# Kernel optimization log

Measured on AMD Instinct MI355X. Metric: run time of the kernel, lower is better.

Reference implementation:

```python
import jax, jax.numpy as jnp
import numpy as np
from jax import lax

B, S, V, E, H = 128, 48, 20000, 620, 2400


def setup_inputs() -> dict:
    key = jax.random.key(0)
    ks = jax.random.split(key, 13)
    s = 0.05
    return {
        "tokens": jax.random.randint(ks[0], (B, S), 0, V),
        "lengths": jax.random.randint(ks[1], (B,), 1, S + 1),
        "emb": jax.random.normal(ks[2], (V, E), jnp.float32) * s,
        "W_ir": jax.random.normal(ks[3], (H, E), jnp.float32) * s,
        "W_ii": jax.random.normal(ks[4], (H, E), jnp.float32) * s,
        "W_in": jax.random.normal(ks[5], (H, E), jnp.float32) * s,
        "b_ir": jax.random.normal(ks[6], (H,), jnp.float32) * s,
        "b_ii": jax.random.normal(ks[7], (H,), jnp.float32) * s,
        "b_in": jax.random.normal(ks[8], (H,), jnp.float32) * s,
        "W_hr": jax.random.normal(ks[9], (H, H), jnp.float32) * s,
        "W_hi": jax.random.normal(ks[10], (H, H), jnp.float32) * s,
        "W_hn": jax.random.normal(ks[11], (H, H), jnp.float32) * s,
    }


def reference(tokens, lengths, emb, W_ir, W_ii, W_in, b_ir, b_ii, b_in, W_hr, W_hi, W_hn):
    x = emb[tokens]  # [B,S,E]
    # Precompute all input-side projections (batched GEMMs): [B,S,H]
    xr = jnp.einsum('bse,he->bsh', x, W_ir) + b_ir
    xi = jnp.einsum('bse,he->bsh', x, W_ii) + b_ii
    xn = jnp.einsum('bse,he->bsh', x, W_in) + b_in

    def step(h, xs):
        xr_t, xi_t, xn_t = xs  # each [B,H]
        r = jax.nn.sigmoid(xr_t + h @ W_hr.T)
        i = jax.nn.sigmoid(xi_t + h @ W_hi.T)
        n = jnp.tanh(xn_t + r * (h @ W_hn.T))
        h_new = (1.0 - i) * n + i * h
        return h_new, h_new

    h0 = jnp.zeros((B, H), x.dtype)
    xs = (xr.swapaxes(0, 1), xi.swapaxes(0, 1), xn.swapaxes(0, 1))  # [S,B,H]
    _, outs = lax.scan(step, h0, xs)
    outs = outs.swapaxes(0, 1)  # [B,S,H]
    # return_last=True: pick hidden at position lengths-1 (mask-mul + sum == gather)
    idx = jnp.clip(lengths - 1, 0, S - 1)
    last = jnp.take_along_axis(outs, idx[:, None, None], axis=1).squeeze(1)  # [B,H]
    return last
```

## Files before the change

### kernel.cpp

```cpp
#include <hip/hip_runtime.h>
#include <stdint.h>
#include <stddef.h>

#define B_  128
#define S_  48
#define E_  620
#define EP  640
#define H_  2400
#define N3  7200
#define KH  2400
#define P1_ITERS 20
#define KZ   5
#define KZI  15
#define UG   48
#define NG   50
#define WCHUNK 512
#define WIT    (9 * WCHUNK)
#define ACH    4096

typedef _Float16 half_t;
typedef __attribute__((ext_vector_type(8))) _Float16 half8;
typedef __attribute__((ext_vector_type(4))) _Float16 half4;
typedef __attribute__((ext_vector_type(4))) float    floatx4;

__device__ __forceinline__ void lds_barrier() {
  __builtin_amdgcn_sched_barrier(0);
  __builtin_amdgcn_s_waitcnt(0xC07F);
  __builtin_amdgcn_s_barrier();
  __builtin_amdgcn_sched_barrier(0);
}

__global__ void gather_cast_x(const int* __restrict__ tokens,
                              const float* __restrict__ emb,
                              half_t* __restrict__ xb) {
  int idx = blockIdx.x * 256 + threadIdx.x;
  int m = idx / EP, c = idx - m * EP;
  float v = 0.f;
  if (c < E_) v = emb[(size_t)tokens[m] * E_ + c];
  xb[idx] = (half_t)v;
}

__global__ void convert_wi(const float* __restrict__ Wir, const float* __restrict__ Wii,
                           const float* __restrict__ Win,
                           const float* __restrict__ bir, const float* __restrict__ bii,
                           const float* __restrict__ bin,
                           half_t* __restrict__ Wi, float* __restrict__ bias) {
  int idx = blockIdx.x * 256 + threadIdx.x;
  int r = idx / EP, c = idx - r * EP;
  const float* W = (r < H_) ? Wir : (r < 2*H_ ? Wii : Win);
  int rr = (r < H_) ? r : (r < 2*H_ ? r - H_ : r - 2*H_);
  float v = (c < E_) ? W[(size_t)rr * E_ + c] : 0.f;
  Wi[idx] = (half_t)v;
  if (c == 0) {
    const float* bb = (r < H_) ? bir : (r < 2*H_ ? bii : bin);
    bias[r] = bb[rr];
  }
}

__global__ void convert_wh(const float* __restrict__ Whr, const float* __restrict__ Whi,
                           const float* __restrict__ Whn, half_t* __restrict__ Wp) {
  int idx = blockIdx.x * 256 + threadIdx.x;
  int r3 = idx / KH, c = idx - r3 * KH;
  const float* W = (r3 < H_) ? Whr : (r3 < 2*H_ ? Whi : Whn);
  int p  = (r3 < H_) ? 0 : (r3 < 2*H_ ? 1 : 2);
  int rr = r3 - p * H_;
  int g = rr / UG, u = rr - g * UG;
  int nw = u >> 4, fm = u & 15;
  int kz = c / 480, kt = (c - kz * 480) >> 5, ksub = c & 31;
  size_t chunk = ((size_t)(g * KZ + kz) * KZI + kt) * 9 + (nw * 3 + p);
  size_t dst = chunk * WCHUNK + ((ksub >> 3) * 16 + fm) * 8 + (ksub & 7);
  Wp[dst] = (half_t)W[(size_t)rr * KH + c];
}

__global__ void init_h(float* __restrict__ h, half_t* __restrict__ Ap) {
  int idx = blockIdx.x * 256 + threadIdx.x;
  h[idx] = 0.f;
  Ap[idx] = (half_t)0.f;
}

__global__ __launch_bounds__(256, 4) void gemm_x(
    const half_t* __restrict__ A,
    const half_t* __restrict__ Bm,
    half_t* __restrict__ C,
    const float* __restrict__ bias)
{
  __shared__ half_t As[2][4096];
  __shared__ half_t Bs[2][4096];

  const int tid = threadIdx.x;
  const int lane = tid & 63;
  const int w = tid >> 6;
  const int m0 = blockIdx.x * 128;
  const int n0 = blockIdx.y * 128;
  const int wm = (w >> 1) * 64, wn = (w & 1) * 64;

  const int c0 = tid, c1 = tid + 256;
  const int rA0 = m0 + (c0 >> 6) * 16 + (c0 & 15), q0 = ((c0 >> 4) & 3) * 8;
  const int rA1 = m0 + (c1 >> 6) * 16 + (c1 & 15), q1 = ((c1 >> 4) & 3) * 8;
  int rB0 = n0 + (c0 >> 6) * 16 + (c0 & 15); if (rB0 >= N3) rB0 = N3 - 1;
  int rB1 = n0 + (c1 >> 6) * 16 + (c1 & 15); if (rB1 >= N3) rB1 = N3 - 1;
  const half_t* pA0 = A  + (size_t)rA0 * EP + q0;
  const half_t* pA1 = A  + (size_t)rA1 * EP + q1;
  const half_t* pB0 = Bm + (size_t)rB0 * EP + q0;
  const half_t* pB1 = Bm + (size_t)rB1 * EP + q1;

  floatx4 acc[4][4] = {};

  half8 ga0 = *(const half8*)(pA0);
  half8 ga1 = *(const half8*)(pA1);
  half8 gb0 = *(const half8*)(pB0);
  half8 gb1 = *(const half8*)(pB1);
  *(half8*)(As[0] + c0 * 8) = ga0;
  *(half8*)(As[0] + c1 * 8) = ga1;
  *(half8*)(Bs[0] + c0 * 8) = gb0;
  *(half8*)(Bs[0] + c1 * 8) = gb1;
  ga0 = *(const half8*)(pA0 + 32);
  ga1 = *(const half8*)(pA1 + 32);
  gb0 = *(const half8*)(pB0 + 32);
  gb1 = *(const half8*)(pB1 + 32);
  lds_barrier();

  #pragma unroll
  for (int i = 0; i < P1_ITERS; ++i) {
    const int cur = i & 1, nxt = cur ^ 1;
    half8 a[4], b[4];
    #pragma unroll
    for (int f = 0; f < 4; ++f) {
      a[f] = *(const half8*)(As[cur] + (((wm >> 4) + f) * 64 + lane) * 8);
      b[f] = *(const half8*)(Bs[cur] + (((wn >> 4) + f) * 64 + lane) * 8);
    }
    if (i + 1 < P1_ITERS) {
      *(half8*)(As[nxt] + c0 * 8) = ga0;
      *(half8*)(As[nxt] + c1 * 8) = ga1;
      *(half8*)(Bs[nxt] + c0 * 8) = gb0;
      *(half8*)(Bs[nxt] + c1 * 8) = gb1;
    }
    if (i + 2 < P1_ITERS) {
      int ko = (i + 2) * 32;
      ga0 = *(const half8*)(pA0 + ko);
      ga1 = *(const half8*)(pA1 + ko);
      gb0 = *(const half8*)(pB0 + ko);
      gb1 = *(const half8*)(pB1 + ko);
    }
    #pragma unroll
    for (int mf = 0; mf < 4; ++mf)
      #pragma unroll
      for (int nf = 0; nf < 4; ++nf)
        acc[mf][nf] = __builtin_amdgcn_mfma_f32_16x16x32_f16(
            a[mf], b[nf], acc[mf][nf], 0, 0, 0);
    if (i + 1 < P1_ITERS) lds_barrier();
  }

  const int col = lane & 15, qr = (lane >> 4) * 4;
  #pragma unroll
  for (int nf = 0; nf < 4; ++nf) {
    int n = n0 + wn + nf * 16 + col;
    if (n >= N3) continue;
    float bv = bias[n];
    #pragma unroll
    for (int mf = 0; mf < 4; ++mf)
      #pragma unroll
      for (int r = 0; r < 4; ++r)
        C[(size_t)(m0 + wm + mf * 16 + qr + r) * N3 + n] =
            (half_t)(acc[mf][nf][r] + bv);
  }
}

__global__ __launch_bounds__(768, 3) void gru_gemm(
    const half_t* __restrict__ Ap_old,
    const half_t* __restrict__ Wp,
    half_t* __restrict__ Gp)
{
  __shared__ half_t S[3][8704];

  const int tid  = threadIdx.x;
  const int lane = tid & 63;
  const int w    = tid >> 6;
  const int mw   = w & 3;
  const int nw   = w >> 2;
  const int g    = blockIdx.x;
  const int kz   = blockIdx.y;

  const half_t* Asrc = Ap_old + (size_t)kz * KZI * ACH;
  const half_t* Wsrc = Wp + (size_t)(g * KZ + kz) * KZI * WIT;

  const bool isA  = tid < 512;
  const bool has1 = tid < 320;
  const half_t* sb0 = isA ? (Asrc + tid * 8) : (Wsrc + (tid - 512) * 8);
  const int     st0 = isA ? ACH : WIT;
  const half_t* sb1 = Wsrc + (tid + 256) * 8;
  const int d0 = tid * 8;
  const int d1 = ACH + (tid + 256) * 8;

  half8 p0 = *(const half8*)(sb0);
  half8 q0{}; if (has1) q0 = *(const half8*)(sb1);
  half8 p1 = *(const half8*)(sb0 + st0);
  half8 q1{}; if (has1) q1 = *(const half8*)(sb1 + WIT);
  *(half8*)(&S[0][d0]) = p0;  if (has1) *(half8*)(&S[0][d1]) = q0;
  *(half8*)(&S[1][d0]) = p1;  if (has1) *(half8*)(&S[1][d1]) = q1;
  half8 rp0 = *(const half8*)(sb0 + 2 * (size_t)st0);
  half8 rq0{}; if (has1) rq0 = *(const half8*)(sb1 + 2 * (size_t)WIT);
  half8 rp1 = *(const half8*)(sb0 + 3 * (size_t)st0);
  half8 rq1{}; if (has1) rq1 = *(const half8*)(sb1 + 3 * (size_t)WIT);
  lds_barrier();

  floatx4 acc[2][3] = {};
  const int aoff0 = (mw * 2 + 0) * 512 + lane * 8;
  const int aoff1 = (mw * 2 + 1) * 512 + lane * 8;
  const int woff  = ACH + nw * 3 * 512 + lane * 8;

  #pragma unroll
  for (int i = 0; i < KZI; ++i) {
    const int cur = i % 3, wb = (i + 2) % 3;
    half8 a0 = *(const half8*)(&S[cur][aoff0]);
    half8 a1 = *(const half8*)(&S[cur][aoff1]);
    half8 b0 = *(const half8*)(&S[cur][woff]);
    half8 b1 = *(const half8*)(&S[cur][woff + 512]);
    half8 b2 = *(const half8*)(&S[cur][woff + 1024]);
    if (i + 2 < KZI) {
      *(half8*)(&S[wb][d0]) = rp0;
      if (has1) *(half8*)(&S[wb][d1]) = rq0;
    }
    rp0 = rp1; rq0 = rq1;
    if (i + 4 < KZI) {
      rp1 = *(const half8*)(sb0 + (size_t)(i + 4) * st0);
      if (has1) rq1 = *(const half8*)(sb1 + (size_t)(i + 4) * WIT);
    }
    acc[0][0] = __builtin_amdgcn_mfma_f32_16x16x32_f16(a0, b0, acc[0][0], 0, 0, 0);
    acc[1][0] = __builtin_amdgcn_mfma_f32_16x16x32_f16(a1, b0, acc[1][0], 0, 0, 0);
    acc[0][1] = __builtin_amdgcn_mfma_f32_16x16x32_f16(a0, b1, acc[0][1], 0, 0, 0);
    acc[1][1] = __builtin_amdgcn_mfma_f32_16x16x32_f16(a1, b1, acc[1][1], 0, 0, 0);
    acc[0][2] = __builtin_amdgcn_mfma_f32_16x16x32_f16(a0, b2, acc[0][2], 0, 0, 0);
    acc[1][2] = __builtin_amdgcn_mfma_f32_16x16x32_f16(a1, b2, acc[1][2], 0, 0, 0);
    if (i + 1 < KZI) lds_barrier();
  }

  const int j  = g * UG + nw * 16 + (lane & 15);
  const int wm = mw * 32;
  const int qr = (lane >> 4) * 4;
  #pragma unroll
  for (int mf = 0; mf < 2; ++mf)
    #pragma unroll
    for (int p = 0; p < 3; ++p)
      #pragma unroll
      for (int r = 0; r < 4; ++r) {
        const int b = wm + mf * 16 + qr + r;
        Gp[((size_t)(kz * B_ + b) * 3 + p) * H_ + j] = (half_t)acc[mf][p][r];
      }
}

__global__ void gru_gate(
    const half_t* __restrict__ Gp,
    const half_t* __restrict__ gx,
    const float* __restrict__ hold,
    float* __restrict__ hnew,
    half_t* __restrict__ Ap_new,
    const int* __restrict__ lengths,
    float* __restrict__ out,
    int t)
{
  const int idx = blockIdx.x * 256 + threadIdx.x;
  const int b = idx / 600;
  const int j = (idx - b * 600) * 4;

  floatx4 G[3] = {};
  #pragma unroll
  for (int kz = 0; kz < KZ; ++kz)
    #pragma unroll
    for (int p = 0; p < 3; ++p) {
      half4 v = *(const half4*)(Gp + ((size_t)(kz * B_ + b) * 3 + p) * H_ + j);
      #pragma unroll
      for (int e = 0; e < 4; ++e) G[p][e] += (float)v[e];
    }

  const size_t rx = ((size_t)b * S_ + t) * N3 + j;
  half4 hxr = *(const half4*)(gx + rx);
  half4 hxi = *(const half4*)(gx + rx + H_);
  half4 hxn = *(const half4*)(gx + rx + 2 * H_);
  floatx4 ho = *(const floatx4*)(hold + (size_t)b * H_ + j);

  floatx4 hv4;
  half4 ap4;
  #pragma unroll
  for (int e = 0; e < 4; ++e) {
    const float rg = 1.f / (1.f + __expf(-((float)hxr[e] + G[0][e])));
    const float ig = 1.f / (1.f + __expf(-((float)hxi[e] + G[1][e])));
    const float ta = (float)hxn[e] + rg * G[2][e];
    const float nn = 1.f - 2.f / (1.f + __expf(2.f * ta));
    hv4[e] = (1.f - ig) * nn + ig * ho[e];
    ap4[e] = (half_t)hv4[e];
  }
  *(floatx4*)(hnew + (size_t)b * H_ + j) = hv4;

  const int kt = j >> 5, ksub = j & 31;
  const int mwb = b >> 5, rb = b & 31, mfb = rb >> 4, fmb = rb & 15;
  const size_t pos = (size_t)kt * ACH + (mwb * 2 + mfb) * 512
                   + ((ksub >> 3) * 16 + fmb) * 8 + (ksub & 7);
  *(half4*)(Ap_new + pos) = ap4;

  int lc = lengths[b] - 1;
  lc = lc < 0 ? 0 : (lc > S_ - 1 ? S_ - 1 : lc);
  if (t == lc) *(floatx4*)(out + (size_t)b * H_ + j) = hv4;
}

extern "C" void kernel_launch(void* const* d_in, const int* in_sizes, int n_in,
                              void* d_out, int out_size, void* d_ws, size_t ws_size,
                              hipStream_t stream)
{
  const int*   tokens  = (const int*)d_in[0];
  const int*   lengths = (const int*)d_in[1];
  const float* emb = (const float*)d_in[2];
  const float* Wir = (const float*)d_in[3];
  const float* Wii = (const float*)d_in[4];
  const float* Win = (const float*)d_in[5];
  const float* bir = (const float*)d_in[6];
  const float* bii = (const float*)d_in[7];
  const float* bin = (const float*)d_in[8];
  const float* Whr = (const float*)d_in[9];
  const float* Whi = (const float*)d_in[10];
  const float* Whn = (const float*)d_in[11];
  float* out = (float*)d_out;

  char* ws = (char*)d_ws;
  size_t off = 0;
  auto alloc = [&](size_t bytes) {
    void* p = ws + off;
    off = (off + bytes + 255) & ~(size_t)255;
    return p;
  };
  half_t* xb   = (half_t*)alloc((size_t)(B_ * S_) * EP * 2);
  half_t* Wi   = (half_t*)alloc((size_t)N3 * EP * 2);
  half_t* Wp   = (half_t*)alloc((size_t)N3 * KH * 2);
  float*  bias = (float*)alloc((size_t)N3 * 4);
  half_t* gx   = (half_t*)alloc((size_t)(B_ * S_) * N3 * 2);
  half_t* Gp   = (half_t*)alloc((size_t)KZ * B_ * N3 * 2);
  float*  h0   = (float*)alloc((size_t)B_ * H_ * 4);
  float*  h1   = (float*)alloc((size_t)B_ * H_ * 4);
  half_t* Ap0  = (half_t*)alloc((size_t)B_ * H_ * 2);
  half_t* Ap1  = (half_t*)alloc((size_t)B_ * H_ * 2);

  gather_cast_x<<<(B_ * S_ * EP) / 256, 256, 0, stream>>>(tokens, emb, xb);
  convert_wi<<<(N3 * EP) / 256, 256, 0, stream>>>(Wir, Wii, Win, bir, bii, bin, Wi, bias);
  convert_wh<<<(N3 * KH) / 256, 256, 0, stream>>>(Whr, Whi, Whn, Wp);
  init_h<<<(B_ * H_) / 256, 256, 0, stream>>>(h0, Ap0);

  gemm_x<<<dim3(48, 57), 256, 0, stream>>>(xb, Wi, gx, bias);

  for (int t = 0; t < S_; ++t) {
    const half_t* ai = (t & 1) ? Ap1 : Ap0;
    half_t*       aw = (t & 1) ? Ap0 : Ap1;
    const float*  ho = (t & 1) ? h1  : h0;
    float*        hn = (t & 1) ? h0  : h1;
    gru_gemm<<<dim3(NG, KZ), 768, 0, stream>>>(ai, Wp, Gp);
    gru_gate<<<(B_ * H_ / 4) / 256, 256, 0, stream>>>(
        Gp, gx, ho, hn, aw, lengths, out, t);
  }
}
```

Before: 1.041 ms.

## Pre-tile input GEMM operands and vectorize conversion and output stores

The conversion kernels now write x and the input weights directly in the per-tile fragment order that gemm_x uses, so each tile's loads become contiguous 16-byte reads instead of strided row gathers. The conversion kernels also process 8 elements per thread with half8 stores, including the recurrent-weight packing. gemm_x's epilogue stages results through shared memory so the output can be written as coalesced half8 rows instead of scattered 2-byte stores. The cost is a larger LDS footprint and an extra staging pass with barriers.

```diff
diff --git a/kernel.cpp b/kernel.cpp
--- a/kernel.cpp
+++ b/kernel.cpp
@@ -17,6 +17,7 @@
 #define WCHUNK 512
 #define WIT    (9 * WCHUNK)
 #define ACH    4096
+#define NBP  57
 
 typedef _Float16 half_t;
 typedef __attribute__((ext_vector_type(8))) _Float16 half8;
@@ -30,46 +31,70 @@
   __builtin_amdgcn_sched_barrier(0);
 }
 
+__device__ __forceinline__ int umap(int mr, int c0) {
+  return ((mr >> 4) << 6) | (((c0 & 31) >> 3) << 4) | (mr & 15);
+}
+
 __global__ void gather_cast_x(const int* __restrict__ tokens,
                               const float* __restrict__ emb,
-                              half_t* __restrict__ xb) {
+                              half_t* __restrict__ xp) {
   int idx = blockIdx.x * 256 + threadIdx.x;
-  int m = idx / EP, c = idx - m * EP;
-  float v = 0.f;
-  if (c < E_) v = emb[(size_t)tokens[m] * E_ + c];
-  xb[idx] = (half_t)v;
+  int m = idx / 80;
+  int c0 = (idx - m * 80) * 8;
+  int tok = tokens[m];
+  half8 v{};
+  #pragma unroll
+  for (int e = 0; e < 8; ++e) {
+    int c = c0 + e;
+    v[e] = (half_t)((c < E_) ? emb[(size_t)tok * E_ + c] : 0.f);
+  }
+  int mb = m >> 7, mr = m & 127, kt = c0 >> 5;
+  *(half8*)(xp + ((size_t)(mb * P1_ITERS + kt) * 512 + umap(mr, c0)) * 8) = v;
 }
 
 __global__ void convert_wi(const float* __restrict__ Wir, const float* __restrict__ Wii,
                            const float* __restrict__ Win,
                            const float* __restrict__ bir, const float* __restrict__ bii,
                            const float* __restrict__ bin,
-                           half_t* __restrict__ Wi, float* __restrict__ bias) {
+                           half_t* __restrict__ Wip, float* __restrict__ bias) {
   int idx = blockIdx.x * 256 + threadIdx.x;
-  int r = idx / EP, c = idx - r * EP;
-  const float* W = (r < H_) ? Wir : (r < 2*H_ ? Wii : Win);
-  int rr = (r < H_) ? r : (r < 2*H_ ? r - H_ : r - 2*H_);
-  float v = (c < E_) ? W[(size_t)rr * E_ + c] : 0.f;
-  Wi[idx] = (half_t)v;
-  if (c == 0) {
-    const float* bb = (r < H_) ? bir : (r < 2*H_ ? bii : bin);
-    bias[r] = bb[rr];
-  }
+  int r = idx / 80;
+  int c0 = (idx - r * 80) * 8;
+  half8 v{};
+  if (r < N3) {
+    const float* W = (r < H_) ? Wir : (r < 2*H_ ? Wii : Win);
+    int rr = (r < H_) ? r : (r < 2*H_ ? r - H_ : r - 2*H_);
+    #pragma unroll
+    for (int e = 0; e < 8; ++e) {
+      int c = c0 + e;
+      v[e] = (half_t)((c < E_) ? W[(size_t)rr * E_ + c] : 0.f);
+    }
+    if (c0 == 0) {
+      const float* bb = (r < H_) ? bir : (r < 2*H_ ? bii : bin);
+      bias[r] = bb[rr];
+    }
+  }
+  int nb = r >> 7, mr = r & 127, kt = c0 >> 5;
+  *(half8*)(Wip + ((size_t)(nb * P1_ITERS + kt) * 512 + umap(mr, c0)) * 8) = v;
 }
 
 __global__ void convert_wh(const float* __restrict__ Whr, const float* __restrict__ Whi,
                            const float* __restrict__ Whn, half_t* __restrict__ Wp) {
   int idx = blockIdx.x * 256 + threadIdx.x;
-  int r3 = idx / KH, c = idx - r3 * KH;
+  if (idx >= N3 * (KH / 8)) return;
+  int r3 = idx / 300;
+  int c0 = (idx - r3 * 300) * 8;
   const float* W = (r3 < H_) ? Whr : (r3 < 2*H_ ? Whi : Whn);
   int p  = (r3 < H_) ? 0 : (r3 < 2*H_ ? 1 : 2);
   int rr = r3 - p * H_;
   int g = rr / UG, u = rr - g * UG;
   int nw = u >> 4, fm = u & 15;
-  int kz = c / 480, kt = (c - kz * 480) >> 5, ksub = c & 31;
+  int kz = c0 / 480, rem = c0 - kz * 480, kt = rem >> 5, ksub = c0 & 31;
+  half8 v;
+  #pragma unroll
+  for (int e = 0; e < 8; ++e) v[e] = (half_t)W[(size_t)rr * KH + c0 + e];
   size_t chunk = ((size_t)(g * KZ + kz) * KZI + kt) * 9 + (nw * 3 + p);
-  size_t dst = chunk * WCHUNK + ((ksub >> 3) * 16 + fm) * 8 + (ksub & 7);
-  Wp[dst] = (half_t)W[(size_t)rr * KH + c];
+  *(half8*)(Wp + chunk * WCHUNK + ((size_t)((ksub >> 3) * 16 + fm)) * 8) = v;
 }
 
 __global__ void init_h(float* __restrict__ h, half_t* __restrict__ Ap) {
@@ -84,8 +109,7 @@
     half_t* __restrict__ C,
     const float* __restrict__ bias)
 {
-  __shared__ half_t As[2][4096];
-  __shared__ half_t Bs[2][4096];
+  __shared__ half_t SH[17408];
 
   const int tid = threadIdx.x;
   const int lane = tid & 63;
@@ -95,14 +119,10 @@
   const int wm = (w >> 1) * 64, wn = (w & 1) * 64;
 
   const int c0 = tid, c1 = tid + 256;
-  const int rA0 = m0 + (c0 >> 6) * 16 + (c0 & 15), q0 = ((c0 >> 4) & 3) * 8;
-  const int rA1 = m0 + (c1 >> 6) * 16 + (c1 & 15), q1 = ((c1 >> 4) & 3) * 8;
-  int rB0 = n0 + (c0 >> 6) * 16 + (c0 & 15); if (rB0 >= N3) rB0 = N3 - 1;
-  int rB1 = n0 + (c1 >> 6) * 16 + (c1 & 15); if (rB1 >= N3) rB1 = N3 - 1;
-  const half_t* pA0 = A  + (size_t)rA0 * EP + q0;
-  const half_t* pA1 = A  + (size_t)rA1 * EP + q1;
-  const half_t* pB0 = Bm + (size_t)rB0 * EP + q0;
-  const half_t* pB1 = Bm + (size_t)rB1 * EP + q1;
+  const half_t* pA0 = A  + ((size_t)blockIdx.x * P1_ITERS * 512 + c0) * 8;
+  const half_t* pA1 = A  + ((size_t)blockIdx.x * P1_ITERS * 512 + c1) * 8;
+  const half_t* pB0 = Bm + ((size_t)blockIdx.y * P1_ITERS * 512 + c0) * 8;
+  const half_t* pB1 = Bm + ((size_t)blockIdx.y * P1_ITERS * 512 + c1) * 8;
 
   floatx4 acc[4][4] = {};
 
@@ -110,14 +130,14 @@
   half8 ga1 = *(const half8*)(pA1);
   half8 gb0 = *(const half8*)(pB0);
   half8 gb1 = *(const half8*)(pB1);
-  *(half8*)(As[0] + c0 * 8) = ga0;
-  *(half8*)(As[0] + c1 * 8) = ga1;
-  *(half8*)(Bs[0] + c0 * 8) = gb0;
-  *(half8*)(Bs[0] + c1 * 8) = gb1;
-  ga0 = *(const half8*)(pA0 + 32);
-  ga1 = *(const half8*)(pA1 + 32);
-  gb0 = *(const half8*)(pB0 + 32);
-  gb1 = *(const half8*)(pB1 + 32);
+  *(half8*)(SH + c0 * 8) = ga0;
+  *(half8*)(SH + c1 * 8) = ga1;
+  *(half8*)(SH + 8192 + c0 * 8) = gb0;
+  *(half8*)(SH + 8192 + c1 * 8) = gb1;
+  ga0 = *(const half8*)(pA0 + 4096);
+  ga1 = *(const half8*)(pA1 + 4096);
+  gb0 = *(const half8*)(pB0 + 4096);
+  gb1 = *(const half8*)(pB1 + 4096);
   lds_barrier();
 
   #pragma unroll
@@ -126,17 +146,17 @@
     half8 a[4], b[4];
     #pragma unroll
     for (int f = 0; f < 4; ++f) {
-      a[f] = *(const half8*)(As[cur] + (((wm >> 4) + f) * 64 + lane) * 8);
-      b[f] = *(const half8*)(Bs[cur] + (((wn >> 4) + f) * 64 + lane) * 8);
+      a[f] = *(const half8*)(SH + cur * 4096 + (((wm >> 4) + f) * 64 + lane) * 8);
+      b[f] = *(const half8*)(SH + 8192 + cur * 4096 + (((wn >> 4) + f) * 64 + lane) * 8);
     }
     if (i + 1 < P1_ITERS) {
-      *(half8*)(As[nxt] + c0 * 8) = ga0;
-      *(half8*)(As[nxt] + c1 * 8) = ga1;
-      *(half8*)(Bs[nxt] + c0 * 8) = gb0;
-      *(half8*)(Bs[nxt] + c1 * 8) = gb1;
+      *(half8*)(SH + nxt * 4096 + c0 * 8) = ga0;
+      *(half8*)(SH + nxt * 4096 + c1 * 8) = ga1;
+      *(half8*)(SH + 8192 + nxt * 4096 + c0 * 8) = gb0;
+      *(half8*)(SH + 8192 + nxt * 4096 + c1 * 8) = gb1;
     }
     if (i + 2 < P1_ITERS) {
-      int ko = (i + 2) * 32;
+      size_t ko = (size_t)(i + 2) * 4096;
       ga0 = *(const half8*)(pA0 + ko);
       ga1 = *(const half8*)(pA1 + ko);
       gb0 = *(const half8*)(pB0 + ko);
@@ -151,18 +171,32 @@
     if (i + 1 < P1_ITERS) lds_barrier();
   }
 
+  __syncthreads();
   const int col = lane & 15, qr = (lane >> 4) * 4;
   #pragma unroll
   for (int nf = 0; nf < 4; ++nf) {
-    int n = n0 + wn + nf * 16 + col;
-    if (n >= N3) continue;
-    float bv = bias[n];
+    const int cloc = wn + nf * 16 + col;
+    const int n = n0 + cloc;
+    const float bv = (n < N3) ? bias[n] : 0.f;
     #pragma unroll
     for (int mf = 0; mf < 4; ++mf)
       #pragma unroll
       for (int r = 0; r < 4; ++r)
-        C[(size_t)(m0 + wm + mf * 16 + qr + r) * N3 + n] =
+        SH[(wm + mf * 16 + qr + r) * 136 + cloc] =
             (half_t)(acc[mf][nf][r] + bv);
+  }
+  __syncthreads();
+  const int row = tid >> 1, cc = (tid & 1) * 64;
+  half_t* crow = C + (size_t)(m0 + row) * N3;
+  #pragma unroll
+  for (int j = 0; j < 8; ++j) {
+    const int nn = n0 + cc + j * 8;
+    half8 vv = *(const half8*)(SH + row * 136 + cc + j * 8);
+    if (nn + 8 <= N3) {
+      *(half8*)(crow + nn) = vv;
+    } else if (nn < N3) {
+      for (int e = 0; e < N3 - nn; ++e) crow[nn + e] = vv[e];
+    }
   }
 }
 
@@ -328,8 +362,8 @@
     off = (off + bytes + 255) & ~(size_t)255;
     return p;
   };
-  half_t* xb   = (half_t*)alloc((size_t)(B_ * S_) * EP * 2);
-  half_t* Wi   = (half_t*)alloc((size_t)N3 * EP * 2);
+  half_t* xp   = (half_t*)alloc((size_t)48 * P1_ITERS * 512 * 8 * 2);
+  half_t* Wip  = (half_t*)alloc((size_t)NBP * P1_ITERS * 512 * 8 * 2);
   half_t* Wp   = (half_t*)alloc((size_t)N3 * KH * 2);
   float*  bias = (float*)alloc((size_t)N3 * 4);
   half_t* gx   = (half_t*)alloc((size_t)(B_ * S_) * N3 * 2);
@@ -339,12 +373,13 @@
   half_t* Ap0  = (half_t*)alloc((size_t)B_ * H_ * 2);
   half_t* Ap1  = (half_t*)alloc((size_t)B_ * H_ * 2);
 
-  gather_cast_x<<<(B_ * S_ * EP) / 256, 256, 0, stream>>>(tokens, emb, xb);
-  convert_wi<<<(N3 * EP) / 256, 256, 0, stream>>>(Wir, Wii, Win, bir, bii, bin, Wi, bias);
-  convert_wh<<<(N3 * KH) / 256, 256, 0, stream>>>(Whr, Whi, Whn, Wp);
+  gather_cast_x<<<(6144 * 80) / 256, 256, 0, stream>>>(tokens, emb, xp);
+  convert_wi<<<(7296 * 80) / 256, 256, 0, stream>>>(Wir, Wii, Win, bir, bii, bin,
+                                                    Wip, bias);
+  convert_wh<<<(N3 * 300 + 255) / 256, 256, 0, stream>>>(Whr, Whi, Whn, Wp);
   init_h<<<(B_ * H_) / 256, 256, 0, stream>>>(h0, Ap0);
 
-  gemm_x<<<dim3(48, 57), 256, 0, stream>>>(xb, Wi, gx, bias);
+  gemm_x<<<dim3(48, NBP), 256, 0, stream>>>(xp, Wip, gx, bias);
 
   for (int t = 0; t < S_; ++t) {
     const half_t* ai = (t & 1) ? Ap1 : Ap0;
```

After: 1.021 ms. About the same (-1.9%).
